# Kernel tuning notes

Measured on AMD Instinct MI355X. Metric: run time of the kernel, lower is better.

## Reference

```python
import jax, jax.numpy as jnp
import numpy as np

B, NQ, NK, C = 16, 8, 4096, 256
H = W = 64
HEADS = 8
CI = 128          # embedding_dim // attention_downsample_rate
HD = CI // HEADS  # per-head dim
EPS = float(np.finfo(np.float32).tiny)


def _gumbel_topk(scores, noise, n):
    # iterative gumbel-softmax top-k relaxation with straight-through hard k-hot
    g = scores + noise
    khot = jnp.zeros_like(g)
    onehot = jnp.zeros_like(g)
    for _ in range(n):
        g = g + jnp.log(jnp.maximum(1.0 - onehot, EPS))
        onehot = jax.nn.softmax(g, axis=-1)
        khot = khot + onehot
    _, ind = jax.lax.top_k(khot, n)
    rows = jnp.arange(khot.shape[0])[:, None]
    hard = jnp.zeros_like(khot).at[rows, ind].set(1.0)
    ret = hard - jax.lax.stop_gradient(khot) + khot  # == hard numerically
    return ret, jnp.sort(ind, axis=1)  # sorted idx = row-major order of boolean-mask select


def _sample_points(pe, content, ret, idx):
    # pe [H,W,C], content [b,H,W,C], ret [b,HW] k-hot, idx [b,k] sorted
    b = ret.shape[0]
    m = ret.reshape(b, H, W, 1)
    pe_m = (pe[None] * m).reshape(b, H * W, -1)
    c_m = (content * m).reshape(b, H * W, -1)
    take = lambda a: jnp.take_along_axis(a, idx[:, :, None], axis=1)
    return take(pe_m), take(c_m)


def _mlp(x, W1, b1, W2, b2, W3, b3):
    x = jax.nn.relu(x @ W1 + b1)
    x = jax.nn.relu(x @ W2 + b2)
    return x @ W3 + b3


def _forward(queries, keys, query_pe, key_pe, guiding_embedding, gumbel_p, gumbel_n,
             static_uncertain, static_refined, Wq, bq, Wk, bk, Wv, bv, Wo, bo,
             uW1, ub1, uW2, ub2, uW3, ub3, rW1, rb1, rW2, rb2, rW3, rb3,
             pe_gauss, point_pos, point_neg, n_sample_points):
    b = queries.shape[0]
    g = guiding_embedding.reshape(b, C, H * W).transpose(0, 2, 1)  # [b, HW, C]
    g = g * keys  # elementwise gating -> new guiding embedding

    # cross attention token -> image (internal dim CI, HEADS heads)
    def split_heads(x, Wx, bx):
        return (x @ Wx + bx).reshape(b, -1, HEADS, HD).transpose(0, 2, 1, 3)
    qh = split_heads(queries + query_pe, Wq, bq)
    kh = split_heads(g + key_pe, Wk, bk)
    vh = split_heads(g, Wv, bv)
    attn = jax.nn.softmax(jnp.einsum('bhqd,bhkd->bhqk', qh, kh) / np.float32(np.sqrt(HD)), axis=-1)
    out = jnp.einsum('bhqk,bhkd->bhqd', attn, vh).transpose(0, 2, 1, 3).reshape(b, -1, CI)
    queries = out @ Wo + bo  # [b, NQ, C]

    q1 = queries[:, 1, :]
    unc_tok = _mlp(jnp.concatenate([jnp.broadcast_to(static_uncertain, (b, C)), q1], -1),
                   uW1, ub1, uW2, ub2, uW3, ub3)
    ref_tok = _mlp(jnp.concatenate([jnp.broadcast_to(static_refined, (b, C)), q1], -1),
                   rW1, rb1, rW2, rb2, rW3, rb3)

    img = g.transpose(0, 2, 1)  # [b, C, HW]
    unc_norm = jax.nn.sigmoid(jnp.einsum('bc,bcn->bn', unc_tok, img))
    ref_mask = jnp.einsum('bc,bcn->bn', ref_tok, img)
    coarse_mask = jnp.einsum('bc,bcn->bn', q1, img)

    queries = jnp.concatenate([queries[:, 0:1], ref_tok[:, None, :], queries[:, 2:]], axis=1)

    # point-sampling reference map + gumbel-softmax top-k (training-path math)
    ref_map = unc_norm * (jax.nn.sigmoid(ref_mask) - jax.nn.sigmoid(coarse_mask))  # [b, HW]
    ret_p, idx_p = _gumbel_topk(ref_map, gumbel_p, n_sample_points)
    ret_n, idx_n = _gumbel_topk(-ref_map, gumbel_n, n_sample_points)

    # random fourier positional encoding of the 64x64 grid (SAM PositionEmbeddingRandom)
    xs = (jnp.arange(W, dtype=jnp.float32) + 0.5) / W
    ys = (jnp.arange(H, dtype=jnp.float32) + 0.5) / H
    coords = jnp.stack([jnp.tile(xs[None, :], (H, 1)), jnp.tile(ys[:, None], (1, W))], axis=-1)
    proj = ((2.0 * coords - 1.0) @ pe_gauss) * np.float32(2.0 * np.pi)  # [H, W, C//2]
    pe = jnp.concatenate([jnp.sin(proj), jnp.cos(proj)], axis=-1)       # [H, W, C]

    # F.interpolate of a 64x64 map to (64,64) is the identity here
    content = (keys + g).reshape(b, H, W, C)

    sp_pe, sp_c = _sample_points(pe, content, ret_p, idx_p)
    sn_pe, sn_c = _sample_points(pe, content, ret_n, idx_n)
    sp_pe = sp_pe + point_pos  # prompt_encoder.point_embeddings[1]
    sn_pe = sn_pe + point_neg  # prompt_encoder.point_embeddings[0]

    query_pe = jnp.concatenate([query_pe, sp_pe, sn_pe], axis=1)
    queries = jnp.concatenate([queries, sp_c, sn_c], axis=1)
    # pack (queries, query_pe) into one array for a single-output reference
    return jnp.concatenate([queries, query_pe], axis=1)  # [b, 2*(NQ+2k), C]


def setup_inputs():
    key = jax.random.key(0)
    ks = iter(jax.random.split(key, 48))
    n = lambda shape, s=1.0: jax.random.normal(next(ks), shape, jnp.float32) * s
    z = lambda shape: jnp.zeros(shape, jnp.float32)
    return {
        'queries': n((B, NQ, C)),
        'keys': n((B, NK, C)),
        'query_pe': n((B, NQ, C)),
        'key_pe': n((B, NK, C)),
        'guiding_embedding': n((B, C, H, W)),
        'gumbel_p': jax.random.gumbel(next(ks), (B, NK), jnp.float32),
        'gumbel_n': jax.random.gumbel(next(ks), (B, NK), jnp.float32),
        'static_uncertain': n((C,), 0.02),
        'static_refined': n((C,), 0.02),
        'Wq': n((C, CI), 0.02), 'bq': z((CI,)),
        'Wk': n((C, CI), 0.02), 'bk': z((CI,)),
        'Wv': n((C, CI), 0.02), 'bv': z((CI,)),
        'Wo': n((CI, C), 0.02), 'bo': z((C,)),
        'uW1': n((2 * C, C // 4), 0.05), 'ub1': z((C // 4,)),
        'uW2': n((C // 4, C // 4), 0.05), 'ub2': z((C // 4,)),
        'uW3': n((C // 4, C), 0.05), 'ub3': z((C,)),
        'rW1': n((2 * C, C // 4), 0.05), 'rb1': z((C // 4,)),
        'rW2': n((C // 4, C // 4), 0.05), 'rb2': z((C // 4,)),
        'rW3': n((C // 4, C), 0.05), 'rb3': z((C,)),
        'pe_gauss': n((2, C // 2)),
        'point_pos': n((C,), 0.02),
        'point_neg': n((C,), 0.02),
        'n_sample_points': 4,
    }


def reference(queries, keys, query_pe, key_pe, guiding_embedding, gumbel_p, gumbel_n,
              static_uncertain, static_refined, Wq, bq, Wk, bk, Wv, bv, Wo, bo,
              uW1, ub1, uW2, ub2, uW3, ub3, rW1, rb1, rW2, rb2, rW3, rb3,
              pe_gauss, point_pos, point_neg, n_sample_points):
    return _forward(queries, keys, query_pe, key_pe, guiding_embedding, gumbel_p, gumbel_n,
                    static_uncertain, static_refined, Wq, bq, Wk, bk, Wv, bv, Wo, bo,
                    uW1, ub1, uW2, ub2, uW3, ub3, rW1, rb1, rW2, rb2, rW3, rb3,
                    pe_gauss, point_pos, point_neg, n_sample_points)
```

## Files before the change

kernel.cpp:

```cpp
#include <hip/hip_runtime.h>

#define BB 16
#define NQn 8
#define NK 4096
#define CC 256
#define NHEADS 8
#define CIn 128
#define HDn 16
#define NHQ 64
#define EPS_TINY 1.17549435e-38f

constexpr size_t OFF_QK   = 0;
constexpr size_t OFF_QBK  = OFF_QK  + (size_t)BB*CC*NHQ;
constexpr size_t OFF_SC   = OFF_QBK + (size_t)BB*NHQ;
constexpr size_t OFF_MP   = OFF_SC  + (size_t)BB*NK*NHQ;
constexpr size_t OFF_SP   = OFF_MP  + (size_t)BB*64*NHQ;
constexpr size_t OFF_M    = OFF_SP  + (size_t)BB*64*NHQ;
constexpr size_t OFF_RS   = OFF_M   + (size_t)BB*NHQ;
constexpr size_t OFF_AVP  = OFF_RS  + (size_t)BB*NHQ;
constexpr size_t OFF_QATT = OFF_AVP + (size_t)BB*16*NHQ*CC;
constexpr size_t OFF_UNC  = OFF_QATT+ (size_t)BB*NQn*CC;
constexpr size_t OFF_REFT = OFF_UNC + (size_t)BB*CC;
constexpr size_t OFF_RMAP = OFF_REFT+ (size_t)BB*CC;
constexpr size_t OFF_IDX  = OFF_RMAP+ (size_t)BB*NK;
constexpr size_t OFF_RV   = OFF_IDX + 128;
constexpr size_t OFF_G    = OFF_RV  + 128;

__global__ __launch_bounds__(256) void k1_qside(
    const float* __restrict__ queries, const float* __restrict__ query_pe,
    const float* __restrict__ Wq, const float* __restrict__ bq,
    const float* __restrict__ Wk, const float* __restrict__ bk,
    float* __restrict__ ws)
{
  int b = blockIdx.x >> 3, q = blockIdx.x & 7, t = threadIdx.x;
  __shared__ float x[CC];
  __shared__ float qh[CIn];
  x[t] = queries[(b*NQn+q)*CC + t] + query_pe[(b*NQn+q)*CC + t];
  __syncthreads();
  if (t < CIn) {
    float a = bq[t];
    for (int c = 0; c < CC; ++c) a += x[c]*Wq[c*CIn + t];
    qh[t] = a * 0.25f;
  }
  __syncthreads();
  float* Qk = ws + OFF_QK;
  #pragma unroll
  for (int h = 0; h < NHEADS; ++h) {
    float a = 0.f;
    #pragma unroll
    for (int d = 0; d < HDn; ++d) a += qh[h*HDn+d] * Wk[t*CIn + h*HDn + d];
    Qk[((size_t)b*CC + t)*NHQ + h*NQn + q] = a;
  }
  if (t < NHEADS) {
    float a = 0.f;
    #pragma unroll
    for (int d = 0; d < HDn; ++d) a += qh[t*HDn+d] * bk[t*HDn+d];
    (ws + OFF_QBK)[b*NHQ + t*NQn + q] = a;
  }
}

__global__ __launch_bounds__(256, 4) void k2_scores(
    const float* __restrict__ keys, const float* __restrict__ key_pe,
    const float* __restrict__ guiding, float* __restrict__ ws)
{
  int b = blockIdx.y, blk = blockIdx.x, n0 = blk * 64, t = threadIdx.x;
  __shared__ __align__(16) float Xs[64][36];
  __shared__ __align__(16) float Qs[32][64];
  __shared__ float Gt[32][66];
  const float* Qk = ws + OFF_QK + (size_t)b*CC*NHQ;
  float* G = ws + OFF_G;
  const int tx = t & 15, ty = t >> 4;
  const int xr = t >> 2, xco = (t & 3) * 8;
  const int gr = (t >> 6) * 8, gn = t & 63;
  const int qc = t >> 3, qh = (t & 7) * 8;
  float acc[4][4] = {};

  float gld[8]; float4 k0v, k1v, p0v, p1v; float qp[8];
  {
    #pragma unroll
    for (int i = 0; i < 8; ++i)
      gld[i] = guiding[((size_t)b*CC + gr + i)*NK + n0 + gn];
    size_t kb = ((size_t)b*NK + n0 + xr)*CC + xco;
    k0v = *(const float4*)&keys[kb];   k1v = *(const float4*)&keys[kb+4];
    p0v = *(const float4*)&key_pe[kb]; p1v = *(const float4*)&key_pe[kb+4];
    #pragma unroll
    for (int i = 0; i < 8; ++i) {
      int l = i*256 + t;
      qp[i] = Qk[(size_t)(l>>6)*NHQ + (l & 63)];
    }
  }
  for (int ch = 0; ch < 8; ++ch) {
    int c0 = ch*32;
    #pragma unroll
    for (int i = 0; i < 8; ++i) Gt[gr + i][gn] = gld[i];
    __syncthreads();
    #pragma unroll
    for (int i = 0; i < 8; ++i) {
      int l = i*256 + t;
      Qs[l>>6][l&63] = qp[i];
    }
    {
      size_t kbase = ((size_t)b*NK + n0 + xr)*CC + c0 + xco;
      float4 g0, g1;
      g0.x = k0v.x * Gt[xco+0][xr]; g0.y = k0v.y * Gt[xco+1][xr];
      g0.z = k0v.z * Gt[xco+2][xr]; g0.w = k0v.w * Gt[xco+3][xr];
      g1.x = k1v.x * Gt[xco+4][xr]; g1.y = k1v.y * Gt[xco+5][xr];
      g1.z = k1v.z * Gt[xco+6][xr]; g1.w = k1v.w * Gt[xco+7][xr];
      *(float4*)&G[kbase]   = g0;
      *(float4*)&G[kbase+4] = g1;
      float4 x0, x1;
      x0.x = g0.x+p0v.x; x0.y = g0.y+p0v.y; x0.z = g0.z+p0v.z; x0.w = g0.w+p0v.w;
      x1.x = g1.x+p1v.x; x1.y = g1.y+p1v.y; x1.z = g1.z+p1v.z; x1.w = g1.w+p1v.w;
      *(float4*)&Xs[xr][xco]   = x0;
      *(float4*)&Xs[xr][xco+4] = x1;
    }
    __syncthreads();
    if (ch < 7) {
      int c1 = c0 + 32;
      #pragma unroll
      for (int i = 0; i < 8; ++i)
        gld[i] = guiding[((size_t)b*CC + c1 + gr + i)*NK + n0 + gn];
      size_t kb2 = ((size_t)b*NK + n0 + xr)*CC + c1 + xco;
      k0v = *(const float4*)&keys[kb2];   k1v = *(const float4*)&keys[kb2+4];
      p0v = *(const float4*)&key_pe[kb2]; p1v = *(const float4*)&key_pe[kb2+4];
      #pragma unroll
      for (int i = 0; i < 8; ++i) {
        int l = i*256 + t;
        qp[i] = Qk[(size_t)(c1 + (l>>6))*NHQ + (l & 63)];
      }
    }
    #pragma unroll 4
    for (int cb = 0; cb < 8; ++cb) {
      float4 xf[4];
      #pragma unroll
      for (int i = 0; i < 4; ++i) xf[i] = *(const float4*)&Xs[4*ty+i][4*cb];
      #pragma unroll
      for (int u = 0; u < 4; ++u) {
        float4 qf = *(const float4*)&Qs[4*cb+u][4*tx];
        float xu[4] = { ((const float*)&xf[0])[u], ((const float*)&xf[1])[u],
                        ((const float*)&xf[2])[u], ((const float*)&xf[3])[u] };
        #pragma unroll
        for (int i = 0; i < 4; ++i) {
          acc[i][0] += xu[i]*qf.x; acc[i][1] += xu[i]*qf.y;
          acc[i][2] += xu[i]*qf.z; acc[i][3] += xu[i]*qf.w;
        }
      }
    }
  }
  const float* qbk = ws + OFF_QBK + (size_t)b*NHQ;
  float qb[4] = {qbk[4*tx], qbk[4*tx+1], qbk[4*tx+2], qbk[4*tx+3]};
  float* scp = ws + OFF_SC + ((size_t)b*NK + n0)*NHQ;
  #pragma unroll
  for (int i = 0; i < 4; ++i) {
    acc[i][0] += qb[0]; acc[i][1] += qb[1]; acc[i][2] += qb[2]; acc[i][3] += qb[3];
    float4 o; o.x = acc[i][0]; o.y = acc[i][1]; o.z = acc[i][2]; o.w = acc[i][3];
    *(float4*)&scp[(size_t)(4*ty + i)*NHQ + 4*tx] = o;
  }
  __syncthreads();
  float* red  = &Qs[0][0];
  float* mfin = &Gt[0][0];
  #pragma unroll
  for (int j = 0; j < 4; ++j) {
    float lm = fmaxf(fmaxf(acc[0][j], acc[1][j]), fmaxf(acc[2][j], acc[3][j]));
    red[ty*64 + 4*tx + j] = lm;
  }
  __syncthreads();
  if (t < 64) {
    float m = red[t];
    #pragma unroll
    for (int r = 1; r < 16; ++r) m = fmaxf(m, red[r*64 + t]);
    mfin[t] = m;
  }
  __syncthreads();
  #pragma unroll
  for (int j = 0; j < 4; ++j) {
    float m = mfin[4*tx + j];
    float ls = expf(acc[0][j]-m) + expf(acc[1][j]-m) + expf(acc[2][j]-m) + expf(acc[3][j]-m);
    red[ty*64 + 4*tx + j] = ls;
  }
  __syncthreads();
  if (t < 64) {
    float s = 0.f;
    #pragma unroll
    for (int r = 0; r < 16; ++r) s += red[r*64 + t];
    (ws + OFF_MP)[((size_t)b*64 + blk)*NHQ + t] = mfin[t];
    (ws + OFF_SP)[((size_t)b*64 + blk)*NHQ + t] = s;
  }
}

__global__ __launch_bounds__(64) void k3b_combine(float* __restrict__ ws)
{
  int b = blockIdx.x, hq = threadIdx.x;
  const float* mp = ws + OFF_MP + (size_t)b*64*NHQ;
  const float* sp = ws + OFF_SP + (size_t)b*64*NHQ;
  float m = -INFINITY;
  #pragma unroll 8
  for (int i = 0; i < 64; ++i) m = fmaxf(m, mp[i*NHQ+hq]);
  float s = 0.f;
  #pragma unroll 8
  for (int i = 0; i < 64; ++i) s += sp[i*NHQ+hq]*expf(mp[i*NHQ+hq]-m);
  (ws+OFF_M)[b*NHQ+hq] = m;
  (ws+OFF_RS)[b*NHQ+hq] = 1.0f/s;
}

__global__ __launch_bounds__(256) void k4_av(float* __restrict__ ws)
{
  int kb = blockIdx.x, ch = blockIdx.y, b = blockIdx.z, t = threadIdx.x;
  int k0 = kb * 256, cbase = ch * 64;
  __shared__ __align__(16) float gld[32][68];
  __shared__ __align__(16) float wld[32][64];
  __shared__ float mv[64], rv[64];
  if (t < 64) { mv[t] = (ws+OFF_M)[b*NHQ+t]; rv[t] = (ws+OFF_RS)[b*NHQ+t]; }
  int hq0 = (t & 15) * 4, c0 = (t >> 4) * 4;
  int sr = t >> 4, sc4 = (t & 15) * 4;
  float accf[4][4] = {};
  const float* sc = ws + OFF_SC;
  const float* G  = ws + OFF_G;
  __syncthreads();
  for (int kk = 0; kk < 256; kk += 32) {
    #pragma unroll
    for (int p = 0; p < 2; ++p)
      *(float4*)&gld[p*16 + sr][sc4] =
        *(const float4*)&G[((size_t)b*NK + k0+kk + p*16 + sr)*CC + cbase + sc4];
    #pragma unroll
    for (int i = 0; i < 8; ++i) {
      int l = i*256 + t; int k = l >> 6, hq = l & 63;
      float v = sc[((size_t)b*NK + k0+kk+k)*NHQ + hq];
      wld[k][hq] = expf(v - mv[hq]) * rv[hq];
    }
    __syncthreads();
    #pragma unroll 4
    for (int k = 0; k < 32; ++k) {
      float4 w4 = *(const float4*)&wld[k][hq0];
      float4 gv = *(const float4*)&gld[k][c0];
      float wq[4] = {w4.x, w4.y, w4.z, w4.w};
      float gq[4] = {gv.x, gv.y, gv.z, gv.w};
      #pragma unroll
      for (int i = 0; i < 4; ++i)
        #pragma unroll
        for (int j = 0; j < 4; ++j) accf[i][j] += wq[i]*gq[j];
    }
    __syncthreads();
  }
  float* avp = ws + OFF_AVP + (((size_t)b*16 + kb)*NHQ)*CC;
  #pragma unroll
  for (int i = 0; i < 4; ++i) {
    float4 o;
    o.x = accf[i][0]; o.y = accf[i][1]; o.z = accf[i][2]; o.w = accf[i][3];
    *(float4*)&avp[(size_t)(hq0 + i)*CC + cbase + c0] = o;
  }
}

__global__ __launch_bounds__(256) void k56_attout(
    const float* __restrict__ Wv, const float* __restrict__ bv,
    const float* __restrict__ Wo, const float* __restrict__ bo,
    float* __restrict__ ws)
{
  int b = blockIdx.x >> 3, q = blockIdx.x & 7, t = threadIdx.x;
  __shared__ float avs[NHEADS][CC];
  __shared__ float outv[CIn];
  const float* avp = ws + OFF_AVP;
  #pragma unroll
  for (int h = 0; h < NHEADS; ++h) {
    int hq = h*NQn + q;
    float a = 0.f;
    #pragma unroll 4
    for (int kb = 0; kb < 16; ++kb)
      a += avp[(((size_t)b*16 + kb)*NHQ + hq)*CC + t];
    avs[h][t] = a;
  }
  __syncthreads();
  if (t < CIn) {
    int h = t >> 4;
    float a = bv[t];
    for (int c = 0; c < CC; ++c) a += avs[h][c]*Wv[c*CIn + t];
    outv[t] = a;
  }
  __syncthreads();
  float a = bo[t];
  for (int ci = 0; ci < CIn; ++ci) a += outv[ci]*Wo[ci*CC + t];
  (ws+OFF_QATT)[((size_t)b*NQn + q)*CC + t] = a;
}

__global__ __launch_bounds__(256) void k7_mlps(
    const float* __restrict__ su, const float* __restrict__ sr,
    const float* __restrict__ uW1, const float* __restrict__ ub1,
    const float* __restrict__ uW2, const float* __restrict__ ub2,
    const float* __restrict__ uW3, const float* __restrict__ ub3,
    const float* __restrict__ rW1, const float* __restrict__ rb1,
    const float* __restrict__ rW2, const float* __restrict__ rb2,
    const float* __restrict__ rW3, const float* __restrict__ rb3,
    float* __restrict__ ws)
{
  int b = blockIdx.x, t = threadIdx.x;
  __shared__ float xs[768];
  __shared__ float h1[2][64], h2[2][64];
  xs[t] = su[t];
  xs[256+t] = (ws+OFF_QATT)[((size_t)b*NQn + 1)*CC + t];
  xs[512+t] = sr[t];
  __syncthreads();
  if (t < 128) {
    int which = t >> 6, o = t & 63;
    const float* W1 = which ? rW1 : uW1;
    const float* b1 = which ? rb1 : ub1;
    int base = which ? 512 : 0;
    float a = b1[o];
    for (int i = 0; i < 256; ++i) a += xs[base+i]*W1[i*64 + o];
    for (int i = 0; i < 256; ++i) a += xs[256+i]*W1[(256+i)*64 + o];
    h1[which][o] = fmaxf(a, 0.f);
  }
  __syncthreads();
  if (t < 128) {
    int which = t >> 6, o = t & 63;
    const float* W2 = which ? rW2 : uW2;
    const float* b2 = which ? rb2 : ub2;
    float a = b2[o];
    #pragma unroll 8
    for (int i = 0; i < 64; ++i) a += h1[which][i]*W2[i*64+o];
    h2[which][o] = fmaxf(a, 0.f);
  }
  __syncthreads();
  {
    float a = ub3[t];
    #pragma unroll 8
    for (int i = 0; i < 64; ++i) a += h2[0][i]*uW3[i*CC + t];
    (ws+OFF_UNC)[b*CC + t] = a;
    float a2 = rb3[t];
    #pragma unroll 8
    for (int i = 0; i < 64; ++i) a2 += h2[1][i]*rW3[i*CC + t];
    (ws+OFF_REFT)[b*CC + t] = a2;
  }
}

__global__ __launch_bounds__(256) void k8_masks(float* __restrict__ ws)
{
  int b = blockIdx.y, t = threadIdx.x;
  int wave = t >> 6, lane = t & 63;
  __shared__ float q1s[CC], us[CC], rts[CC];
  q1s[t] = (ws+OFF_QATT)[((size_t)b*NQn+1)*CC + t];
  us[t]  = (ws+OFF_UNC)[b*CC + t];
  rts[t] = (ws+OFF_REFT)[b*CC + t];
  __syncthreads();
  float q1v[4], usv[4], rtv[4];
  #pragma unroll
  for (int u = 0; u < 4; ++u) {
    q1v[u] = q1s[lane*4+u]; usv[u] = us[lane*4+u]; rtv[u] = rts[lane*4+u];
  }
  const float* G = ws + OFF_G;
  float* rmap = ws + OFF_RMAP + (size_t)b*NK;
  int n_base = blockIdx.x*32 + wave*8;
  for (int r = 0; r < 8; ++r) {
    int n = n_base + r;
    float4 gv = *(const float4*)&G[((size_t)b*NK + n)*CC + lane*4];
    float aq = gv.x*q1v[0] + gv.y*q1v[1] + gv.z*q1v[2] + gv.w*q1v[3];
    float au = gv.x*usv[0] + gv.y*usv[1] + gv.z*usv[2] + gv.w*usv[3];
    float ar = gv.x*rtv[0] + gv.y*rtv[1] + gv.z*rtv[2] + gv.w*rtv[3];
    #pragma unroll
    for (int s = 1; s < 64; s <<= 1) {
      aq += __shfl_xor(aq, s, 64);
      au += __shfl_xor(au, s, 64);
      ar += __shfl_xor(ar, s, 64);
    }
    if (lane == 0) {
      float un = 1.f/(1.f+expf(-au));
      rmap[n] = un * (1.f/(1.f+expf(-ar)) - 1.f/(1.f+expf(-aq)));
    }
  }
}

__global__ __launch_bounds__(256) void k9_gumbel(
    const float* __restrict__ gp, const float* __restrict__ gn,
    float* __restrict__ ws)
{
  int sign = blockIdx.x, b = blockIdx.y, t = threadIdx.x;
  int wave = t >> 6, lane = t & 63;
  const float* noise = sign ? gn : gp;
  const float* rmap = ws + OFF_RMAP + (size_t)b*NK;
  float g[16], kh[16], oh[16];
  #pragma unroll
  for (int i = 0; i < 16; ++i) {
    int n = i*256 + t;
    float scv = rmap[n];
    if (sign) scv = -scv;
    g[i] = scv + noise[(size_t)b*NK + n];
    kh[i] = 0.f; oh[i] = 0.f;
  }
  __shared__ float wred[8];
  __shared__ float selV[16];
  __shared__ int   selIdx[16];
  for (int it = 0; it < 4; ++it) {
    if (it > 0) {
      #pragma unroll
      for (int i = 0; i < 16; ++i) g[i] += logf(fmaxf(1.f - oh[i], EPS_TINY));
    }
    float m = g[0];
    #pragma unroll
    for (int i = 1; i < 16; ++i) m = fmaxf(m, g[i]);
    #pragma unroll
    for (int s = 1; s < 64; s <<= 1) m = fmaxf(m, __shfl_xor(m, s, 64));
    if (lane == 0) wred[wave] = m;
    __syncthreads();
    m = fmaxf(fmaxf(wred[0], wred[1]), fmaxf(wred[2], wred[3]));
    float e[16], ls = 0.f;
    #pragma unroll
    for (int i = 0; i < 16; ++i) { e[i] = expf(g[i]-m); ls += e[i]; }
    #pragma unroll
    for (int s = 1; s < 64; s <<= 1) ls += __shfl_xor(ls, s, 64);
    if (lane == 0) wred[4+wave] = ls;
    __syncthreads();
    float ssum = wred[4]+wred[5]+wred[6]+wred[7];
    #pragma unroll
    for (int i = 0; i < 16; ++i) { oh[i] = e[i]/ssum; kh[i] += oh[i]; }
  }
  int id[4]; float rr[4];
  for (int j = 0; j < 4; ++j) {
    float bv = kh[0]; int bi = t;
    #pragma unroll
    for (int i = 1; i < 16; ++i) {
      if (kh[i] > bv) { bv = kh[i]; bi = i*256 + t; }
    }
    #pragma unroll
    for (int s = 1; s < 64; s <<= 1) {
      float ov = __shfl_xor(bv, s, 64);
      int   oi = __shfl_xor(bi, s, 64);
      if (ov > bv || (ov == bv && oi < bi)) { bv = ov; bi = oi; }
    }
    if (lane == 0) { selV[j*4+wave] = bv; selIdx[j*4+wave] = bi; }
    __syncthreads();
    bv = selV[j*4]; bi = selIdx[j*4];
    #pragma unroll
    for (int w = 1; w < 4; ++w) {
      float ov = selV[j*4+w]; int oi = selIdx[j*4+w];
      if (ov > bv || (ov == bv && oi < bi)) { bv = ov; bi = oi; }
    }
    id[j] = bi; rr[j] = (1.f - bv) + bv;
    if ((bi & 255) == t) kh[bi >> 8] = -1.f;
  }
  if (t == 0) {
    for (int a = 0; a < 3; ++a)
      for (int c2 = a+1; c2 < 4; ++c2)
        if (id[c2] < id[a]) { int ti=id[a]; id[a]=id[c2]; id[c2]=ti; float tr=rr[a]; rr[a]=rr[c2]; rr[c2]=tr; }
    int* iout = (int*)(ws + OFF_IDX);
    float* rout = ws + OFF_RV;
    for (int j = 0; j < 4; ++j) {
      iout[(sign*BB + b)*4 + j] = id[j];
      rout[(sign*BB + b)*4 + j] = rr[j];
    }
  }
}

__global__ __launch_bounds__(256) void k10_out(
    const float* __restrict__ keys, const float* __restrict__ query_pe,
    const float* __restrict__ point_pos, const float* __restrict__ point_neg,
    const float* __restrict__ pe_gauss,
    float* __restrict__ ws, float* __restrict__ out)
{
  int b = blockIdx.y, r = blockIdx.x, t = threadIdx.x;
  const float* G = ws + OFF_G;
  float val;
  if (r < 8) {
    val = (r == 1) ? (ws+OFF_REFT)[b*CC + t]
                   : (ws+OFF_QATT)[((size_t)b*NQn + r)*CC + t];
  } else if (r < 16) {
    int j = r - 8; int sign = j >> 2; int jj = j & 3;
    int idx = ((const int*)(ws+OFF_IDX))[(sign*BB + b)*4 + jj];
    float rvv = (ws+OFF_RV)[(sign*BB + b)*4 + jj];
    float kv = keys[((size_t)b*NK + idx)*CC + t];
    float gv = G[((size_t)b*NK + idx)*CC + t];
    val = (kv + gv) * rvv;
  } else if (r < 24) {
    val = query_pe[((size_t)b*NQn + (r-16))*CC + t];
  } else {
    int j = r - 24; int sign = j >> 2; int jj = j & 3;
    int idx = ((const int*)(ws+OFF_IDX))[(sign*BB + b)*4 + jj];
    float rvv = (ws+OFF_RV)[(sign*BB + b)*4 + jj];
    const float* point = sign ? point_neg : point_pos;
    int h = idx >> 6, w = idx & 63;
    float x = (w + 0.5f)/64.f, y = (h + 0.5f)/64.f;
    int jf = (t < 128) ? t : (t - 128);
    float proj = ((2.f*x - 1.f)*pe_gauss[jf] + (2.f*y - 1.f)*pe_gauss[128 + jf]) * 6.28318530717958647692f;
    float sv = (t < 128) ? sinf(proj) : cosf(proj);
    val = sv*rvv + point[t];
  }
  out[((size_t)b*32 + r)*CC + t] = val;
}

extern "C" void kernel_launch(void* const* d_in, const int* in_sizes, int n_in,
                              void* d_out, int out_size, void* d_ws, size_t ws_size,
                              hipStream_t stream)
{
  const float* queries   = (const float*)d_in[0];
  const float* keys      = (const float*)d_in[1];
  const float* query_pe  = (const float*)d_in[2];
  const float* key_pe    = (const float*)d_in[3];
  const float* guiding   = (const float*)d_in[4];
  const float* gumbel_p  = (const float*)d_in[5];
  const float* gumbel_n  = (const float*)d_in[6];
  const float* s_unc     = (const float*)d_in[7];
  const float* s_ref     = (const float*)d_in[8];
  const float* Wq  = (const float*)d_in[9];   const float* bq  = (const float*)d_in[10];
  const float* Wk  = (const float*)d_in[11];  const float* bk  = (const float*)d_in[12];
  const float* Wv  = (const float*)d_in[13];  const float* bv  = (const float*)d_in[14];
  const float* Wo  = (const float*)d_in[15];  const float* bo  = (const float*)d_in[16];
  const float* uW1 = (const float*)d_in[17];  const float* ub1 = (const float*)d_in[18];
  const float* uW2 = (const float*)d_in[19];  const float* ub2 = (const float*)d_in[20];
  const float* uW3 = (const float*)d_in[21];  const float* ub3 = (const float*)d_in[22];
  const float* rW1 = (const float*)d_in[23];  const float* rb1 = (const float*)d_in[24];
  const float* rW2 = (const float*)d_in[25];  const float* rb2 = (const float*)d_in[26];
  const float* rW3 = (const float*)d_in[27];  const float* rb3 = (const float*)d_in[28];
  const float* pe_gauss  = (const float*)d_in[29];
  const float* point_pos = (const float*)d_in[30];
  const float* point_neg = (const float*)d_in[31];
  float* ws = (float*)d_ws;
  float* out = (float*)d_out;

  k1_qside  <<<dim3(BB*NQn),    256, 0, stream>>>(queries, query_pe, Wq, bq, Wk, bk, ws);
  k2_scores <<<dim3(64, BB),    256, 0, stream>>>(keys, key_pe, guiding, ws);
  k3b_combine<<<dim3(BB),        64, 0, stream>>>(ws);
  k4_av     <<<dim3(16, 4, BB), 256, 0, stream>>>(ws);
  k56_attout<<<dim3(BB*NQn),    256, 0, stream>>>(Wv, bv, Wo, bo, ws);
  k7_mlps   <<<dim3(BB),        256, 0, stream>>>(s_unc, s_ref, uW1, ub1, uW2, ub2, uW3, ub3,
                                                  rW1, rb1, rW2, rb2, rW3, rb3, ws);
  k8_masks  <<<dim3(128, BB),   256, 0, stream>>>(ws);
  k9_gumbel <<<dim3(2, BB),     256, 0, stream>>>(gumbel_p, gumbel_n, ws);
  k10_out   <<<dim3(32, BB),    256, 0, stream>>>(keys, query_pe, point_pos, point_neg,
                                                  pe_gauss, ws, out);
}
```

Before: 211.7 us.

## Restructure AV kernel with register prefetch, fuse attout with MLPs, widen gumbel block

k4_av now has one 512-thread block cover all 256 channels of a 256-key chunk, so the grid loses its channel dimension and the softmax weights are exponentiated once per chunk instead of once per channel slice. It also prefetches the next 32-key slice of G and the scores into registers while the current slice is being computed. The MLP kernel is folded into the attention-output kernel, with the q==1 block reusing its result directly, which removes one launch and one global round-trip. k9_gumbel moves to 512 threads with fewer elements per thread, trading shorter per-thread work for larger cross-wave reductions and fewer blocks in k4.

Result: slower. 232.5 us (+9.9%).

```diff
diff --git a/kernel.cpp b/kernel.cpp
--- a/kernel.cpp
+++ b/kernel.cpp
@@ -72,7 +72,6 @@
   const int tx = t & 15, ty = t >> 4;
   const int xr = t >> 2, xco = (t & 3) * 8;
   const int gr = (t >> 6) * 8, gn = t & 63;
-  const int qc = t >> 3, qh = (t & 7) * 8;
   float acc[4][4] = {};
 
   float gld[8]; float4 k0v, k1v, p0v, p1v; float qp[8];
@@ -203,86 +202,75 @@
   (ws+OFF_RS)[b*NHQ+hq] = 1.0f/s;
 }
 
-__global__ __launch_bounds__(256) void k4_av(float* __restrict__ ws)
-{
-  int kb = blockIdx.x, ch = blockIdx.y, b = blockIdx.z, t = threadIdx.x;
-  int k0 = kb * 256, cbase = ch * 64;
-  __shared__ __align__(16) float gld[32][68];
-  __shared__ __align__(16) float wld[32][64];
+__global__ __launch_bounds__(512) void k4_av(float* __restrict__ ws)
+{
+  int kb = blockIdx.x, b = blockIdx.y, t = threadIdx.x;
+  int k0 = kb * 256;
+  int wv = t >> 6, lane = t & 63;
+  int hqb = wv * 8, c0 = lane * 4;
+  __shared__ __align__(16) float gld[32][260];
+  __shared__ __align__(16) float wld[32][68];
   __shared__ float mv[64], rv[64];
   if (t < 64) { mv[t] = (ws+OFF_M)[b*NHQ+t]; rv[t] = (ws+OFF_RS)[b*NHQ+t]; }
-  int hq0 = (t & 15) * 4, c0 = (t >> 4) * 4;
-  int sr = t >> 4, sc4 = (t & 15) * 4;
-  float accf[4][4] = {};
-  const float* sc = ws + OFF_SC;
+  const float* scp = ws + OFF_SC;
   const float* G  = ws + OFF_G;
+  const int sr = t >> 4, scb = (t & 15) * 4;
+  float acc[8][4] = {};
+  float4 gp[4]; float wp[4];
+  #pragma unroll
+  for (int p = 0; p < 4; ++p)
+    gp[p] = *(const float4*)&G[((size_t)b*NK + k0 + sr)*CC + scb + p*64];
+  #pragma unroll
+  for (int i = 0; i < 4; ++i) {
+    int l = i*512 + t;
+    wp[i] = scp[((size_t)b*NK + k0 + (l>>6))*NHQ + (l&63)];
+  }
   __syncthreads();
   for (int kk = 0; kk < 256; kk += 32) {
     #pragma unroll
-    for (int p = 0; p < 2; ++p)
-      *(float4*)&gld[p*16 + sr][sc4] =
-        *(const float4*)&G[((size_t)b*NK + k0+kk + p*16 + sr)*CC + cbase + sc4];
-    #pragma unroll
-    for (int i = 0; i < 8; ++i) {
-      int l = i*256 + t; int k = l >> 6, hq = l & 63;
-      float v = sc[((size_t)b*NK + k0+kk+k)*NHQ + hq];
-      wld[k][hq] = expf(v - mv[hq]) * rv[hq];
-    }
-    __syncthreads();
-    #pragma unroll 4
+    for (int p = 0; p < 4; ++p)
+      *(float4*)&gld[sr][scb + p*64] = gp[p];
+    #pragma unroll
+    for (int i = 0; i < 4; ++i) {
+      int l = i*512 + t; int k = l >> 6, hq = l & 63;
+      wld[k][hq] = expf(wp[i] - mv[hq]) * rv[hq];
+    }
+    __syncthreads();
+    if (kk + 32 < 256) {
+      #pragma unroll
+      for (int p = 0; p < 4; ++p)
+        gp[p] = *(const float4*)&G[((size_t)b*NK + k0+kk+32 + sr)*CC + scb + p*64];
+      #pragma unroll
+      for (int i = 0; i < 4; ++i) {
+        int l = i*512 + t;
+        wp[i] = scp[((size_t)b*NK + k0+kk+32 + (l>>6))*NHQ + (l&63)];
+      }
+    }
+    #pragma unroll 2
     for (int k = 0; k < 32; ++k) {
-      float4 w4 = *(const float4*)&wld[k][hq0];
-      float4 gv = *(const float4*)&gld[k][c0];
-      float wq[4] = {w4.x, w4.y, w4.z, w4.w};
-      float gq[4] = {gv.x, gv.y, gv.z, gv.w};
-      #pragma unroll
-      for (int i = 0; i < 4; ++i)
-        #pragma unroll
-        for (int j = 0; j < 4; ++j) accf[i][j] += wq[i]*gq[j];
+      float4 g4 = *(const float4*)&gld[k][c0];
+      float4 w0 = *(const float4*)&wld[k][hqb];
+      float4 w1 = *(const float4*)&wld[k][hqb+4];
+      float wq[8] = {w0.x,w0.y,w0.z,w0.w, w1.x,w1.y,w1.z,w1.w};
+      #pragma unroll
+      for (int i = 0; i < 8; ++i) {
+        acc[i][0] += wq[i]*g4.x; acc[i][1] += wq[i]*g4.y;
+        acc[i][2] += wq[i]*g4.z; acc[i][3] += wq[i]*g4.w;
+      }
     }
     __syncthreads();
   }
   float* avp = ws + OFF_AVP + (((size_t)b*16 + kb)*NHQ)*CC;
   #pragma unroll
-  for (int i = 0; i < 4; ++i) {
-    float4 o;
-    o.x = accf[i][0]; o.y = accf[i][1]; o.z = accf[i][2]; o.w = accf[i][3];
-    *(float4*)&avp[(size_t)(hq0 + i)*CC + cbase + c0] = o;
+  for (int i = 0; i < 8; ++i) {
+    float4 o; o.x=acc[i][0]; o.y=acc[i][1]; o.z=acc[i][2]; o.w=acc[i][3];
+    *(float4*)&avp[(size_t)(hqb + i)*CC + c0] = o;
   }
 }
 
 __global__ __launch_bounds__(256) void k56_attout(
     const float* __restrict__ Wv, const float* __restrict__ bv,
     const float* __restrict__ Wo, const float* __restrict__ bo,
-    float* __restrict__ ws)
-{
-  int b = blockIdx.x >> 3, q = blockIdx.x & 7, t = threadIdx.x;
-  __shared__ float avs[NHEADS][CC];
-  __shared__ float outv[CIn];
-  const float* avp = ws + OFF_AVP;
-  #pragma unroll
-  for (int h = 0; h < NHEADS; ++h) {
-    int hq = h*NQn + q;
-    float a = 0.f;
-    #pragma unroll 4
-    for (int kb = 0; kb < 16; ++kb)
-      a += avp[(((size_t)b*16 + kb)*NHQ + hq)*CC + t];
-    avs[h][t] = a;
-  }
-  __syncthreads();
-  if (t < CIn) {
-    int h = t >> 4;
-    float a = bv[t];
-    for (int c = 0; c < CC; ++c) a += avs[h][c]*Wv[c*CIn + t];
-    outv[t] = a;
-  }
-  __syncthreads();
-  float a = bo[t];
-  for (int ci = 0; ci < CIn; ++ci) a += outv[ci]*Wo[ci*CC + t];
-  (ws+OFF_QATT)[((size_t)b*NQn + q)*CC + t] = a;
-}
-
-__global__ __launch_bounds__(256) void k7_mlps(
     const float* __restrict__ su, const float* __restrict__ sr,
     const float* __restrict__ uW1, const float* __restrict__ ub1,
     const float* __restrict__ uW2, const float* __restrict__ ub2,
@@ -292,11 +280,36 @@
     const float* __restrict__ rW3, const float* __restrict__ rb3,
     float* __restrict__ ws)
 {
-  int b = blockIdx.x, t = threadIdx.x;
+  int b = blockIdx.x >> 3, q = blockIdx.x & 7, t = threadIdx.x;
+  __shared__ float avs[NHEADS][CC];
+  __shared__ float outv[CIn];
   __shared__ float xs[768];
   __shared__ float h1[2][64], h2[2][64];
+  const float* avp = ws + OFF_AVP;
+  #pragma unroll
+  for (int h = 0; h < NHEADS; ++h) {
+    int hq = h*NQn + q;
+    float a = 0.f;
+    #pragma unroll 4
+    for (int kb = 0; kb < 16; ++kb)
+      a += avp[(((size_t)b*16 + kb)*NHQ + hq)*CC + t];
+    avs[h][t] = a;
+  }
+  __syncthreads();
+  if (t < CIn) {
+    int h = t >> 4;
+    float a = bv[t];
+    for (int c = 0; c < CC; ++c) a += avs[h][c]*Wv[c*CIn + t];
+    outv[t] = a;
+  }
+  __syncthreads();
+  float a = bo[t];
+  for (int ci = 0; ci < CIn; ++ci) a += outv[ci]*Wo[ci*CC + t];
+  (ws+OFF_QATT)[((size_t)b*NQn + q)*CC + t] = a;
+
+  if (q != 1) return;
   xs[t] = su[t];
-  xs[256+t] = (ws+OFF_QATT)[((size_t)b*NQn + 1)*CC + t];
+  xs[256+t] = a;
   xs[512+t] = sr[t];
   __syncthreads();
   if (t < 128) {
@@ -304,31 +317,31 @@
     const float* W1 = which ? rW1 : uW1;
     const float* b1 = which ? rb1 : ub1;
     int base = which ? 512 : 0;
-    float a = b1[o];
-    for (int i = 0; i < 256; ++i) a += xs[base+i]*W1[i*64 + o];
-    for (int i = 0; i < 256; ++i) a += xs[256+i]*W1[(256+i)*64 + o];
-    h1[which][o] = fmaxf(a, 0.f);
+    float acc1 = b1[o];
+    for (int i = 0; i < 256; ++i) acc1 += xs[base+i]*W1[i*64 + o];
+    for (int i = 0; i < 256; ++i) acc1 += xs[256+i]*W1[(256+i)*64 + o];
+    h1[which][o] = fmaxf(acc1, 0.f);
   }
   __syncthreads();
   if (t < 128) {
     int which = t >> 6, o = t & 63;
     const float* W2 = which ? rW2 : uW2;
     const float* b2 = which ? rb2 : ub2;
-    float a = b2[o];
+    float acc2 = b2[o];
     #pragma unroll 8
-    for (int i = 0; i < 64; ++i) a += h1[which][i]*W2[i*64+o];
-    h2[which][o] = fmaxf(a, 0.f);
+    for (int i = 0; i < 64; ++i) acc2 += h1[which][i]*W2[i*64+o];
+    h2[which][o] = fmaxf(acc2, 0.f);
   }
   __syncthreads();
   {
-    float a = ub3[t];
+    float au = ub3[t];
     #pragma unroll 8
-    for (int i = 0; i < 64; ++i) a += h2[0][i]*uW3[i*CC + t];
-    (ws+OFF_UNC)[b*CC + t] = a;
-    float a2 = rb3[t];
+    for (int i = 0; i < 64; ++i) au += h2[0][i]*uW3[i*CC + t];
+    (ws+OFF_UNC)[b*CC + t] = au;
+    float ar = rb3[t];
     #pragma unroll 8
-    for (int i = 0; i < 64; ++i) a2 += h2[1][i]*rW3[i*CC + t];
-    (ws+OFF_REFT)[b*CC + t] = a2;
+    for (int i = 0; i < 64; ++i) ar += h2[1][i]*rW3[i*CC + t];
+    (ws+OFF_REFT)[b*CC + t] = ar;
   }
 }
 
@@ -368,7 +381,7 @@
   }
 }
 
-__global__ __launch_bounds__(256) void k9_gumbel(
+__global__ __launch_bounds__(512) void k9_gumbel(
     const float* __restrict__ gp, const float* __restrict__ gn,
     float* __restrict__ ws)
 {
@@ -376,48 +389,52 @@
   int wave = t >> 6, lane = t & 63;
   const float* noise = sign ? gn : gp;
   const float* rmap = ws + OFF_RMAP + (size_t)b*NK;
-  float g[16], kh[16], oh[16];
-  #pragma unroll
-  for (int i = 0; i < 16; ++i) {
-    int n = i*256 + t;
+  float g[8], kh[8], oh[8];
+  #pragma unroll
+  for (int i = 0; i < 8; ++i) {
+    int n = i*512 + t;
     float scv = rmap[n];
     if (sign) scv = -scv;
     g[i] = scv + noise[(size_t)b*NK + n];
     kh[i] = 0.f; oh[i] = 0.f;
   }
-  __shared__ float wred[8];
-  __shared__ float selV[16];
-  __shared__ int   selIdx[16];
+  __shared__ float wred[16];
+  __shared__ float selV[32];
+  __shared__ int   selIdx[32];
   for (int it = 0; it < 4; ++it) {
     if (it > 0) {
       #pragma unroll
-      for (int i = 0; i < 16; ++i) g[i] += logf(fmaxf(1.f - oh[i], EPS_TINY));
+      for (int i = 0; i < 8; ++i) g[i] += logf(fmaxf(1.f - oh[i], EPS_TINY));
     }
     float m = g[0];
     #pragma unroll
-    for (int i = 1; i < 16; ++i) m = fmaxf(m, g[i]);
+    for (int i = 1; i < 8; ++i) m = fmaxf(m, g[i]);
     #pragma unroll
     for (int s = 1; s < 64; s <<= 1) m = fmaxf(m, __shfl_xor(m, s, 64));
     if (lane == 0) wred[wave] = m;
     __syncthreads();
-    m = fmaxf(fmaxf(wred[0], wred[1]), fmaxf(wred[2], wred[3]));
-    float e[16], ls = 0.f;
-    #pragma unroll
-    for (int i = 0; i < 16; ++i) { e[i] = expf(g[i]-m); ls += e[i]; }
+    m = wred[0];
+    #pragma unroll
+    for (int w = 1; w < 8; ++w) m = fmaxf(m, wred[w]);
+    float e[8], ls = 0.f;
+    #pragma unroll
+    for (int i = 0; i < 8; ++i) { e[i] = expf(g[i]-m); ls += e[i]; }
     #pragma unroll
     for (int s = 1; s < 64; s <<= 1) ls += __shfl_xor(ls, s, 64);
-    if (lane == 0) wred[4+wave] = ls;
-    __syncthreads();
-    float ssum = wred[4]+wred[5]+wred[6]+wred[7];
-    #pragma unroll
-    for (int i = 0; i < 16; ++i) { oh[i] = e[i]/ssum; kh[i] += oh[i]; }
+    if (lane == 0) wred[8+wave] = ls;
+    __syncthreads();
+    float ssum = wred[8];
+    #pragma unroll
+    for (int w = 1; w < 8; ++w) ssum += wred[8+w];
+    #pragma unroll
+    for (int i = 0; i < 8; ++i) { oh[i] = e[i]/ssum; kh[i] += oh[i]; }
   }
   int id[4]; float rr[4];
   for (int j = 0; j < 4; ++j) {
     float bv = kh[0]; int bi = t;
     #pragma unroll
-    for (int i = 1; i < 16; ++i) {
-      if (kh[i] > bv) { bv = kh[i]; bi = i*256 + t; }
+    for (int i = 1; i < 8; ++i) {
+      if (kh[i] > bv) { bv = kh[i]; bi = i*512 + t; }
     }
     #pragma unroll
     for (int s = 1; s < 64; s <<= 1) {
@@ -425,16 +442,16 @@
       int   oi = __shfl_xor(bi, s, 64);
       if (ov > bv || (ov == bv && oi < bi)) { bv = ov; bi = oi; }
     }
-    if (lane == 0) { selV[j*4+wave] = bv; selIdx[j*4+wave] = bi; }
-    __syncthreads();
-    bv = selV[j*4]; bi = selIdx[j*4];
-    #pragma unroll
-    for (int w = 1; w < 4; ++w) {
-      float ov = selV[j*4+w]; int oi = selIdx[j*4+w];
+    if (lane == 0) { selV[j*8+wave] = bv; selIdx[j*8+wave] = bi; }
+    __syncthreads();
+    bv = selV[j*8]; bi = selIdx[j*8];
+    #pragma unroll
+    for (int w = 1; w < 8; ++w) {
+      float ov = selV[j*8+w]; int oi = selIdx[j*8+w];
       if (ov > bv || (ov == bv && oi < bi)) { bv = ov; bi = oi; }
     }
     id[j] = bi; rr[j] = (1.f - bv) + bv;
-    if ((bi & 255) == t) kh[bi >> 8] = -1.f;
+    if ((bi & 511) == t) kh[bi >> 9] = -1.f;
   }
   if (t == 0) {
     for (int a = 0; a < 3; ++a)
@@ -517,12 +534,13 @@
   k1_qside  <<<dim3(BB*NQn),    256, 0, stream>>>(queries, query_pe, Wq, bq, Wk, bk, ws);
   k2_scores <<<dim3(64, BB),    256, 0, stream>>>(keys, key_pe, guiding, ws);
   k3b_combine<<<dim3(BB),        64, 0, stream>>>(ws);
-  k4_av     <<<dim3(16, 4, BB), 256, 0, stream>>>(ws);
-  k56_attout<<<dim3(BB*NQn),    256, 0, stream>>>(Wv, bv, Wo, bo, ws);
-  k7_mlps   <<<dim3(BB),        256, 0, stream>>>(s_unc, s_ref, uW1, ub1, uW2, ub2, uW3, ub3,
+  k4_av     <<<dim3(16, BB),    512, 0, stream>>>(ws);
+  k56_attout<<<dim3(BB*NQn),    256, 0, stream>>>(Wv, bv, Wo, bo,
+                                                  s_unc, s_ref,
+                                                  uW1, ub1, uW2, ub2, uW3, ub3,
                                                   rW1, rb1, rW2, rb2, rW3, rb3, ws);
   k8_masks  <<<dim3(128, BB),   256, 0, stream>>>(ws);
-  k9_gumbel <<<dim3(2, BB),     256, 0, stream>>>(gumbel_p, gumbel_n, ws);
+  k9_gumbel <<<dim3(2, BB),     512, 0, stream>>>(gumbel_p, gumbel_n, ws);
   k10_out   <<<dim3(32, BB),    256, 0, stream>>>(keys, query_pe, point_pos, point_neg,
                                                   pe_gauss, ws, out);
 }
```
